# Performance work log

Hardware: AMD Instinct MI355X
Metric: run time of the kernel (lower is better)

The kernel has to match this reference:

```python
import jax, jax.numpy as jnp
import numpy as np

EPS = 1e-6


def setup_inputs() -> dict:
    key = jax.random.key(0)
    k = jax.random.split(key, 6)
    B, C_in, C_out, H, W, E = 32, 256, 256, 64, 64, 1024
    x = jax.random.normal(k[0], (B, C_in, H, W), dtype=jnp.float32)
    emb = jax.random.normal(k[1], (B, E), dtype=jnp.float32)
    # adaLN Linear(E -> 2*C_in). (Module zero-inits these; random here for coverage.)
    ada_w = jax.random.normal(k[2], (2 * C_in, E), dtype=jnp.float32) * 0.02
    ada_b = jax.random.normal(k[3], (2 * C_in,), dtype=jnp.float32) * 0.02
    # 1x1 Conv2d(C_in -> C_out) weight (C_out, C_in) and bias
    conv_w = jax.random.normal(k[4], (C_out, C_in), dtype=jnp.float32) * (1.0 / np.sqrt(C_in))
    conv_b = jax.random.normal(k[5], (C_out,), dtype=jnp.float32) * 0.02
    return {"x": x, "emb": emb, "ada_w": ada_w, "ada_b": ada_b,
            "conv_w": conv_w, "conv_b": conv_b}


def reference(x, emb, ada_w, ada_b, conv_w, conv_b):
    # adaLN modulation: SiLU(emb) @ W^T + b -> (B, 2C) -> shift, scale
    mod = jax.nn.silu(emb) @ ada_w.T + ada_b          # (B, 2C)
    shift, scale = jnp.split(mod, 2, axis=1)          # each (B, C)
    # RMSNorm over channel dim (no affine)
    rms = jax.lax.rsqrt(jnp.mean(x * x, axis=1, keepdims=True) + EPS)  # (B,1,H,W)
    xn = x * rms
    # modulate: x * (1 + scale) + shift, broadcast over H,W
    xm = xn * (1.0 + scale[:, :, None, None]) + shift[:, :, None, None]
    # 1x1 conv == channel GEMM
    y = jnp.einsum('bchw,oc->bohw', xm, conv_w) + conv_b[None, :, None, None]
    return jax.nn.selu(y)
```

## Files before the change

kernel.cpp:

```cpp
#include <hip/hip_runtime.h>
#include <hip/hip_bf16.h>

typedef __attribute__((ext_vector_type(4))) float f32x4;
typedef __attribute__((ext_vector_type(8))) short s16x8;
typedef __attribute__((ext_vector_type(4))) unsigned short u16x4;

__device__ __forceinline__ unsigned short f2bf(float f) {
  unsigned u = __builtin_bit_cast(unsigned, f);
  u += 0x7fffu + ((u >> 16) & 1u);
  return (unsigned short)(u >> 16);
}

__global__ __launch_bounds__(512) void k_mod(const float* __restrict__ emb,
                                             const float* __restrict__ ada_w,
                                             const float* __restrict__ ada_b,
                                             float* __restrict__ mod) {
  __shared__ __align__(16) float semb[32][1028];
  const int t = threadIdx.x;
  for (int i = t; i < 8192; i += 512) {
    f32x4 v = ((const f32x4*)emb)[i];
    f32x4 s;
#pragma unroll
    for (int j = 0; j < 4; ++j) s[j] = v[j] / (1.f + __expf(-v[j]));
    *(f32x4*)&semb[i >> 8][(i & 255) << 2] = s;
  }
  __syncthreads();
  const int jl = t >> 5, b = t & 31;
  const int j = blockIdx.x * 16 + jl;
  const f32x4* aw = (const f32x4*)(ada_w + (size_t)j * 1024);
  float acc = 0.f;
  for (int q = 0; q < 256; ++q) {
    f32x4 a = aw[q];
    f32x4 sv = *(const f32x4*)&semb[b][q * 4];
    acc += a[0] * sv[0] + a[1] * sv[1] + a[2] * sv[2] + a[3] * sv[3];
  }
  mod[b * 512 + j] = acc + ada_b[j];
}

__global__ __launch_bounds__(256) void k_prep(const float* __restrict__ mod,
                                              const float* __restrict__ conv_w,
                                              const float* __restrict__ conv_b,
                                              unsigned short* __restrict__ wp,
                                              float* __restrict__ dvec) {
  const int b = blockIdx.y;
  const int o = blockIdx.x * 4 + (threadIdx.x >> 6);
  const int l = threadIdx.x & 63;
  const float* sh = mod + b * 512;
  const float* sc = mod + b * 512 + 256;
  f32x4 cw = ((const f32x4*)(conv_w + (size_t)o * 256))[l];
  f32x4 s4 = ((const f32x4*)sc)[l];
  f32x4 h4 = ((const f32x4*)sh)[l];
  u16x4 wq;
#pragma unroll
  for (int j = 0; j < 4; ++j) wq[j] = f2bf(cw[j] * (1.f + s4[j]));
  const int wr = o >> 6, m = (o >> 4) & 3, lr = o & 15;
  const int kk = l >> 3, g = (l >> 1) & 3, jb = 4 * (l & 1);
  *(u16x4*)(wp + (size_t)b * 65536 + (((wr * 4 + m) * 8 + kk) * 512 + g * 128 + lr * 8 + jb)) = wq;
  float dd = cw[0] * h4[0] + cw[1] * h4[1] + cw[2] * h4[2] + cw[3] * h4[3];
#pragma unroll
  for (int off = 32; off; off >>= 1) dd += __shfl_down(dd, off);
  if (l == 0) dvec[b * 256 + o] = dd + conv_b[o];
}

__global__ __launch_bounds__(512, 4) void k_main(const float* __restrict__ x,
                                                 const unsigned short* __restrict__ wp,
                                                 const float* __restrict__ dvec,
                                                 float* __restrict__ out) {
  constexpr int HW = 4096;
  __shared__ __align__(16) unsigned short lds_bt[64 * 256];
  __shared__ float lds_part[8][64];
  __shared__ float lds_rms[64];
  __shared__ float lds_d[256];

  const int t = threadIdx.x;
  const int b = blockIdx.y;
  const int s0 = blockIdx.x * 64;
  const int w = t >> 6, lane = t & 63;
  const int wr = w >> 1, wc = w & 1;
  const int lr = lane & 15, g = lane >> 4;

  const unsigned short* A2 = wp + (size_t)b * 65536;

  if (t < 256) lds_d[t] = dvec[b * 256 + t];

  const float* xb = x + (size_t)b * (256 * HW) + s0;
  const int sq = t & 15, cg = t >> 4;
  f32x4 sacc = {0.f, 0.f, 0.f, 0.f};
#pragma unroll
  for (int it = 0; it < 8; ++it) {
    int c = cg + 32 * it;
    f32x4 v = *(const f32x4*)(xb + (size_t)c * HW + 4 * sq);
    sacc += v * v;
#pragma unroll
    for (int r = 0; r < 4; ++r) {
      int s = 4 * sq + r;
      lds_bt[s * 256 + (c ^ (((s >> 1) & 7) << 3))] = f2bf(v[r]);
    }
  }
#pragma unroll
  for (int off = 16; off <= 32; off <<= 1) {
#pragma unroll
    for (int j = 0; j < 4; ++j) sacc[j] += __shfl_xor(sacc[j], off);
  }
  if (lane < 16) *(f32x4*)&lds_part[w][4 * sq] = sacc;
  __syncthreads();
  if (t < 64) {
    float sum = 0.f;
#pragma unroll
    for (int q = 0; q < 8; ++q) sum += lds_part[q][t];
    lds_rms[t] = rsqrtf(sum * (1.0f / 256.0f) + 1e-6f);
  }
  __syncthreads();

  f32x4 acc[4][2] = {};
  const int sA = 32 * wc + lr;
  const int sB = sA + 16;

#pragma unroll
  for (int kk = 0; kk < 8; ++kk) {
    s16x8 af[4];
#pragma unroll
    for (int m = 0; m < 4; ++m)
      af[m] = *(const s16x8*)(A2 + (((wr * 4 + m) * 8 + kk) * 512 + lane * 8));

    const int c0 = kk * 32 + g * 8;
    s16x8 b0 = *(const s16x8*)&lds_bt[sA * 256 + (c0 ^ (((sA >> 1) & 7) << 3))];
    s16x8 b1 = *(const s16x8*)&lds_bt[sB * 256 + (c0 ^ (((sB >> 1) & 7) << 3))];

#pragma unroll
    for (int m = 0; m < 4; ++m) {
      acc[m][0] = __builtin_amdgcn_mfma_f32_16x16x32_bf16(af[m], b0, acc[m][0], 0, 0, 0);
      acc[m][1] = __builtin_amdgcn_mfma_f32_16x16x32_bf16(af[m], b1, acc[m][1], 0, 0, 0);
    }
  }

  float* ob = out + (size_t)b * (256 * HW) + s0;
#pragma unroll
  for (int m = 0; m < 4; ++m) {
    const int o0 = 64 * wr + 16 * m + 4 * g;
#pragma unroll
    for (int n = 0; n < 2; ++n) {
      const int s = 32 * wc + 16 * n + lr;
      const float rr = lds_rms[s];
#pragma unroll
      for (int r = 0; r < 4; ++r) {
        float v = rr * acc[m][n][r] + lds_d[o0 + r];
        float res = v > 0.f ? 1.0507009873554805f * v
                            : 1.7580993408473766f * expm1f(v);
        ob[(size_t)(o0 + r) * HW + s] = res;
      }
    }
  }
}

extern "C" void kernel_launch(void* const* d_in, const int* in_sizes, int n_in,
                              void* d_out, int out_size, void* d_ws, size_t ws_size,
                              hipStream_t stream) {
  const float* x      = (const float*)d_in[0];
  const float* emb    = (const float*)d_in[1];
  const float* ada_w  = (const float*)d_in[2];
  const float* ada_b  = (const float*)d_in[3];
  const float* conv_w = (const float*)d_in[4];
  const float* conv_b = (const float*)d_in[5];
  float* out = (float*)d_out;

  float* mod  = (float*)d_ws;
  float* dvec = mod + 32 * 512;
  unsigned short* wp = (unsigned short*)(dvec + 32 * 256);

  k_mod<<<dim3(32), 512, 0, stream>>>(emb, ada_w, ada_b, mod);
  k_prep<<<dim3(64, 32), 256, 0, stream>>>(mod, conv_w, conv_b, wp, dvec);
  k_main<<<dim3(64, 32), 512, 0, stream>>>(x, wp, dvec, out);
}
```

Before: 101.0 us.

## Pipeline x tiles via async global-to-LDS loads with larger spatial tiles

The main kernel now streams x in fp32 through double-buffered LDS using global_load_lds, 32 channels at a time, and overlaps the loads with MFMA work. Each block covers 256 spatial positions instead of 64, so each block reuses the per-batch weights over a larger tile. The RMS sum and the bf16 conversion now happen inside the K loop. The launch grid shrinks to 512 blocks and launch bounds drop to two blocks per CU. Costs: more accumulator registers (32 f32x4), per-element bf16 conversion on LDS reads that may bank-conflict, and lower occupancy.

```diff
diff --git a/kernel.cpp b/kernel.cpp
--- a/kernel.cpp
+++ b/kernel.cpp
@@ -62,92 +62,105 @@
   if (l == 0) dvec[b * 256 + o] = dd + conv_b[o];
 }
 
-__global__ __launch_bounds__(512, 4) void k_main(const float* __restrict__ x,
+__global__ __launch_bounds__(512, 2) void k_main(const float* __restrict__ x,
                                                  const unsigned short* __restrict__ wp,
                                                  const float* __restrict__ dvec,
                                                  float* __restrict__ out) {
   constexpr int HW = 4096;
-  __shared__ __align__(16) unsigned short lds_bt[64 * 256];
-  __shared__ float lds_part[8][64];
-  __shared__ float lds_rms[64];
-  __shared__ float lds_d[256];
+  __shared__ __align__(16) float xf[2][32][256];
+  __shared__ float prt[2][256];
+  __shared__ float rms[256];
 
   const int t = threadIdx.x;
   const int b = blockIdx.y;
-  const int s0 = blockIdx.x * 64;
+  const int s0 = blockIdx.x * 256;
   const int w = t >> 6, lane = t & 63;
   const int wr = w >> 1, wc = w & 1;
   const int lr = lane & 15, g = lane >> 4;
 
+  const float* xb = x + (size_t)b * (256 * HW) + s0;
   const unsigned short* A2 = wp + (size_t)b * 65536;
 
-  if (t < 256) lds_d[t] = dvec[b * 256 + t];
+#define ISSUE(K, BUF)                                                                     \
+  {                                                                                       \
+    _Pragma("unroll") for (int i = 0; i < 4; ++i) {                                       \
+      const float* gp = xb + (size_t)((K)*32 + w * 4 + i) * HW + lane * 4;                \
+      void* lp = (void*)&xf[BUF][w * 4 + i][0];                                           \
+      __builtin_amdgcn_global_load_lds((const __attribute__((address_space(1))) void*)gp, \
+                                       (__attribute__((address_space(3))) void*)lp, 16,   \
+                                       0, 0);                                             \
+    }                                                                                     \
+  }
 
-  const float* xb = x + (size_t)b * (256 * HW) + s0;
-  const int sq = t & 15, cg = t >> 4;
-  f32x4 sacc = {0.f, 0.f, 0.f, 0.f};
+  ISSUE(0, 0);
+  ISSUE(1, 1);
+
+  const int sS = t & 255, ch = t >> 8;
+  float rs = 0.f;
+  f32x4 acc[4][8];
 #pragma unroll
-  for (int it = 0; it < 8; ++it) {
-    int c = cg + 32 * it;
-    f32x4 v = *(const f32x4*)(xb + (size_t)c * HW + 4 * sq);
-    sacc += v * v;
+  for (int m = 0; m < 4; ++m)
 #pragma unroll
-    for (int r = 0; r < 4; ++r) {
-      int s = 4 * sq + r;
-      lds_bt[s * 256 + (c ^ (((s >> 1) & 7) << 3))] = f2bf(v[r]);
-    }
-  }
-#pragma unroll
-  for (int off = 16; off <= 32; off <<= 1) {
-#pragma unroll
-    for (int j = 0; j < 4; ++j) sacc[j] += __shfl_xor(sacc[j], off);
-  }
-  if (lane < 16) *(f32x4*)&lds_part[w][4 * sq] = sacc;
-  __syncthreads();
-  if (t < 64) {
-    float sum = 0.f;
-#pragma unroll
-    for (int q = 0; q < 8; ++q) sum += lds_part[q][t];
-    lds_rms[t] = rsqrtf(sum * (1.0f / 256.0f) + 1e-6f);
-  }
-  __syncthreads();
-
-  f32x4 acc[4][2] = {};
-  const int sA = 32 * wc + lr;
-  const int sB = sA + 16;
+    for (int n = 0; n < 8; ++n) acc[m][n] = f32x4{0.f, 0.f, 0.f, 0.f};
 
 #pragma unroll
-  for (int kk = 0; kk < 8; ++kk) {
+  for (int k = 0; k < 8; ++k) {
+    const int buf = k & 1;
+    if (k < 7) {
+      asm volatile("s_waitcnt vmcnt(4)" ::: "memory");
+    } else {
+      asm volatile("s_waitcnt vmcnt(0)" ::: "memory");
+    }
+    __builtin_amdgcn_s_barrier();
+
+#pragma unroll
+    for (int i = 0; i < 16; ++i) {
+      float v = xf[buf][ch * 16 + i][sS];
+      rs += v * v;
+    }
+
     s16x8 af[4];
 #pragma unroll
     for (int m = 0; m < 4; ++m)
-      af[m] = *(const s16x8*)(A2 + (((wr * 4 + m) * 8 + kk) * 512 + lane * 8));
+      af[m] = *(const s16x8*)(A2 + (((wr * 4 + m) * 8 + k) * 512 + lane * 8));
+#pragma unroll
+    for (int n = 0; n < 8; ++n) {
+      const int s = 128 * wc + 16 * n + lr;
+      s16x8 bf;
+#pragma unroll
+      for (int j = 0; j < 8; ++j) bf[j] = (short)f2bf(xf[buf][g * 8 + j][s]);
+#pragma unroll
+      for (int m = 0; m < 4; ++m)
+        acc[m][n] = __builtin_amdgcn_mfma_f32_16x16x32_bf16(af[m], bf, acc[m][n], 0, 0, 0);
+    }
 
-    const int c0 = kk * 32 + g * 8;
-    s16x8 b0 = *(const s16x8*)&lds_bt[sA * 256 + (c0 ^ (((sA >> 1) & 7) << 3))];
-    s16x8 b1 = *(const s16x8*)&lds_bt[sB * 256 + (c0 ^ (((sB >> 1) & 7) << 3))];
+    asm volatile("s_waitcnt lgkmcnt(0)" ::: "memory");
+    __builtin_amdgcn_s_barrier();
+    if (k < 6) ISSUE(k + 2, buf);
+  }
+#undef ISSUE
 
+  prt[ch][sS] = rs;
+  __syncthreads();
+  if (t < 256) rms[t] = rsqrtf((prt[0][t] + prt[1][t]) * (1.0f / 256.0f) + 1e-6f);
+  __syncthreads();
+
+  float rr[8];
 #pragma unroll
-    for (int m = 0; m < 4; ++m) {
-      acc[m][0] = __builtin_amdgcn_mfma_f32_16x16x32_bf16(af[m], b0, acc[m][0], 0, 0, 0);
-      acc[m][1] = __builtin_amdgcn_mfma_f32_16x16x32_bf16(af[m], b1, acc[m][1], 0, 0, 0);
-    }
-  }
-
+  for (int n = 0; n < 8; ++n) rr[n] = rms[128 * wc + 16 * n + lr];
   float* ob = out + (size_t)b * (256 * HW) + s0;
 #pragma unroll
   for (int m = 0; m < 4; ++m) {
     const int o0 = 64 * wr + 16 * m + 4 * g;
+    const f32x4 dv = *(const f32x4*)(dvec + (size_t)b * 256 + o0);
 #pragma unroll
-    for (int n = 0; n < 2; ++n) {
-      const int s = 32 * wc + 16 * n + lr;
-      const float rr = lds_rms[s];
+    for (int n = 0; n < 8; ++n) {
 #pragma unroll
       for (int r = 0; r < 4; ++r) {
-        float v = rr * acc[m][n][r] + lds_d[o0 + r];
+        float v = rr[n] * acc[m][n][r] + dv[r];
         float res = v > 0.f ? 1.0507009873554805f * v
-                            : 1.7580993408473766f * expm1f(v);
-        ob[(size_t)(o0 + r) * HW + s] = res;
+                            : 1.7580993408473766f * (__expf(v) - 1.f);
+        ob[(size_t)(o0 + r) * HW + 128 * wc + 16 * n + lr] = res;
       }
     }
   }
@@ -170,5 +183,5 @@
 
   k_mod<<<dim3(32), 512, 0, stream>>>(emb, ada_w, ada_b, mod);
   k_prep<<<dim3(64, 32), 256, 0, stream>>>(mod, conv_w, conv_b, wp, dvec);
-  k_main<<<dim3(64, 32), 512, 0, stream>>>(x, wp, dvec, out);
+  k_main<<<dim3(16, 32), 512, 0, stream>>>(x, wp, dvec, out);
 }
```

Measured after the change: 102.8 us. Within noise of the previous version (+1.8%).
